# Kernel tuning notes

Hardware: AMD Instinct MI355X
Metric: run time of the kernel (lower is better)

## Reference

```python
import jax, jax.numpy as jnp
import numpy as np

E = 8            # num_experts
PS = 8           # patch size (fixed across layers since ps-2 < 8)
F = 6            # fourier frequencies
CC = 4 + 8 * F   # coord feature channels = 52
RH = 16          # router hidden channels (embed_dim)
TEMP = 1.0
THRESH = 0.05
LAYERS = [(3, 8), (8, 16), (16, 16), (16, 32)]  # (C_in, C_out) per layer
NUM_CLASSES = 100


def coord_features(H, W, ps, nf):
    # [4+8F, H, W]: global (x,y) + patch-local (x,y) + sin/cos fourier bands
    gy = (jnp.arange(H, dtype=jnp.float32) + 0.5) / H
    gx = (jnp.arange(W, dtype=jnp.float32) + 0.5) / W
    ly = ((jnp.arange(H) % ps).astype(jnp.float32) + 0.5) / ps
    lx = ((jnp.arange(W) % ps).astype(jnp.float32) + 0.5) / ps
    Gy = jnp.broadcast_to(gy[:, None], (H, W))
    Gx = jnp.broadcast_to(gx[None, :], (H, W))
    Ly = jnp.broadcast_to(ly[:, None], (H, W))
    Lx = jnp.broadcast_to(lx[None, :], (H, W))
    base = jnp.stack([Gx, Gy, Lx, Ly], 0)  # [4,H,W]
    bands = [base]
    for f in range(nf):
        w = (2.0 ** f) * jnp.pi
        bands.append(jnp.sin(w * base))
        bands.append(jnp.cos(w * base))
    return jnp.concatenate(bands, 0)


def patchify(x, ps):
    B, C, H, W = x.shape
    h, w = H // ps, W // ps
    x = x.reshape(B, C, h, ps, w, ps).transpose(0, 2, 4, 1, 3, 5)
    return x.reshape(B, h * w, C, ps, ps), h, w


def unpatchify(x, h, w):
    # 'b (h w) c ph pw -> b c (h ph) (w pw)'
    B, P, C, ph, pw = x.shape
    return x.reshape(B, h, w, C, ph, pw).transpose(0, 3, 1, 4, 2, 5).reshape(B, C, h * ph, w * pw)


def pce_layer(X, ew, eb, rw, rb, rlw, rlb):
    B, C, H, W = X.shape
    Xp, h, w = patchify(X, PS)             # [B,P,C,ps,ps]
    P = h * w
    Xf = Xp.reshape(B * P, C, PS, PS)
    coords = coord_features(H, W, PS, F)   # [CC,H,W] (same for every image)
    Cp, _, _ = patchify(coords[None], PS)
    Cp = Cp[0]                             # [P,CC,ps,ps]
    # Router: 1x1 conv proj -> ReLU -> global avg pool -> linear -> softmax/temp -> threshold + renorm
    z = jax.nn.relu(jnp.einsum('rc,pcij->prij', rw, Cp) + rb[None, :, None, None])
    z = z.mean((2, 3))                     # [P,RH]
    logits = z @ rlw.T + rlb               # [P,E]
    probs = jax.nn.softmax(logits / TEMP, axis=-1)
    keep = (probs >= THRESH).astype(probs.dtype)
    probs = probs * keep
    probs = probs / (probs.sum(-1, keepdims=True) + 1e-9)
    scores = jnp.broadcast_to(probs[None], (B, P, E))  # [B,P,E]
    # Dense all-experts conv: stack experts along output channels of one conv
    y = jax.lax.conv_general_dilated(Xf, ew, (1, 1), 'SAME',
                                     dimension_numbers=('NCHW', 'OIHW', 'NCHW'))
    y = jax.nn.relu(y + eb[None, :, None, None])       # [B*P, E*Cout, ps, ps]
    Cout = ew.shape[0] // E
    y = y.reshape(B, P, E, Cout, PS, PS)
    out = jnp.einsum('bpecij,bpe->bpcij', y, scores)   # weighted combine over experts
    return unpatchify(out, h, w)


def setup_inputs() -> dict:
    key = jax.random.key(0)
    ks = jax.random.split(key, 32)
    d = {'X': jax.random.normal(ks[0], (16, 3, 128, 128), dtype=jnp.float32)}
    ki = 1
    for li, (cin, cout) in enumerate(LAYERS):
        d[f'ew{li}'] = jax.random.normal(ks[ki], (E * cout, cin, 3, 3), dtype=jnp.float32) * (1.0 / np.sqrt(cin * 9)); ki += 1
        d[f'eb{li}'] = jax.random.normal(ks[ki], (E * cout,), dtype=jnp.float32) * 0.01; ki += 1
        d[f'rw{li}'] = jax.random.normal(ks[ki], (RH, CC), dtype=jnp.float32) * (1.0 / np.sqrt(CC)); ki += 1
        d[f'rb{li}'] = jax.random.normal(ks[ki], (RH,), dtype=jnp.float32) * 0.01; ki += 1
        d[f'rlw{li}'] = jax.random.normal(ks[ki], (E, RH), dtype=jnp.float32) * (1.0 / np.sqrt(RH)); ki += 1
        d[f'rlb{li}'] = jax.random.normal(ks[ki], (E,), dtype=jnp.float32) * 0.01; ki += 1
    d['fcw'] = jax.random.normal(ks[ki], (NUM_CLASSES, LAYERS[-1][1] * 8 * 8), dtype=jnp.float32) * 0.02; ki += 1
    d['fcb'] = jnp.zeros((NUM_CLASSES,), dtype=jnp.float32)
    return d


def reference(X, ew0, eb0, rw0, rb0, rlw0, rlb0,
              ew1, eb1, rw1, rb1, rlw1, rlb1,
              ew2, eb2, rw2, rb2, rlw2, rlb2,
              ew3, eb3, rw3, rb3, rlw3, rlb3,
              fcw, fcb):
    layer_params = [(ew0, eb0, rw0, rb0, rlw0, rlb0),
                    (ew1, eb1, rw1, rb1, rlw1, rlb1),
                    (ew2, eb2, rw2, rb2, rlw2, rlb2),
                    (ew3, eb3, rw3, rb3, rlw3, rlb3)]
    for p in layer_params:
        X = pce_layer(X, *p)
    B, C, H, W = X.shape
    # AdaptiveAvgPool2d(8): exact 16x16 mean pooling for 128x128
    pooled = X.reshape(B, C, 8, H // 8, 8, W // 8).mean((3, 5))
    flat = pooled.reshape(B, -1)
    return flat @ fcw.T + fcb
```

## Files before the change

kernel.cpp:

```cpp
#include <hip/hip_runtime.h>
#include <math.h>

#define NE 8
#define PI_F 3.14159265358979323846f

typedef _Float16 half8 __attribute__((ext_vector_type(8)));
typedef float f32x4 __attribute__((ext_vector_type(4)));
typedef unsigned int uint2v __attribute__((ext_vector_type(2)));
typedef unsigned int u32x4 __attribute__((ext_vector_type(4)));
typedef unsigned short u16x4 __attribute__((ext_vector_type(4)));

#define CP 24
#define ROWS 240
#define NELEM 2400

__device__ __forceinline__ unsigned short f2h_bits(float v) {
    union { _Float16 h; unsigned short u; } cv;
    cv.h = (_Float16)v;
    return cv.u;
}

struct SetupArgs {
    const float* rw[4]; const float* rb[4]; const float* rlw[4]; const float* rlb[4];
    const float* ew[4];
    float* probs;
    unsigned short* w0; unsigned short* w1; unsigned short* w2; unsigned short* w3;
};

template<int CIN, int COUT_R, int COUT_P, int CSTR, int KS>
__device__ __forceinline__ void prep_one(
    const float* __restrict__ ew, unsigned short* __restrict__ wA, int idx)
{
    int j    = idx & 7;
    int lane = (idx >> 3) & 63;
    int t2   = idx >> 9;
    int ks   = t2 % KS;
    int mt   = t2 / KS;
    int m    = mt * 16 + (lane & 15);
    int e    = m / COUT_P, row = m % COUT_P;
    int k    = ks * 32 + (lane >> 4) * 8 + j;
    int cin  = k % CSTR, r = k / CSTR;
    float val = 0.0f;
    if (row < COUT_R && cin < CIN && r < 9)
        val = ew[((size_t)(e * COUT_R + row) * CIN + cin) * 9 + r];
    wA[idx] = f2h_bits(val);
}

__global__ __launch_bounds__(256) void setup_all(SetupArgs sa)
{
    int bx = blockIdx.x, tid = threadIdx.x;
    if (bx < 256) {
        int layer = tid >> 6, lane = tid & 63;
        const float* rw  = sa.rw[layer];  const float* rb  = sa.rb[layer];
        const float* rlw = sa.rlw[layer]; const float* rlb = sa.rlb[layer];
        int p = bx, py = p >> 4, px = p & 15;
        int i = lane >> 3, j = lane & 7;
        int y = py * 8 + i, x = px * 8 + j;

        float base0 = (x + 0.5f) / 128.0f;
        float base1 = (y + 0.5f) / 128.0f;
        float base2 = (j + 0.5f) / 8.0f;
        float base3 = (i + 0.5f) / 8.0f;

        float coord[52];
        coord[0] = base0; coord[1] = base1; coord[2] = base2; coord[3] = base3;
        int c = 4;
        #pragma unroll
        for (int f = 0; f < 6; ++f) {
            float w = PI_F * (float)(1 << f);
            coord[c+0] = sinf(w * base0); coord[c+1] = sinf(w * base1);
            coord[c+2] = sinf(w * base2); coord[c+3] = sinf(w * base3);
            coord[c+4] = cosf(w * base0); coord[c+5] = cosf(w * base1);
            coord[c+6] = cosf(w * base2); coord[c+7] = cosf(w * base3);
            c += 8;
        }
        float z[16];
        #pragma unroll
        for (int r = 0; r < 16; ++r) {
            float a = rb[r];
            #pragma unroll
            for (int cc = 0; cc < 52; ++cc) a += rw[r*52 + cc] * coord[cc];
            z[r] = fmaxf(a, 0.0f);
        }
        #pragma unroll
        for (int r = 0; r < 16; ++r) {
            float v = z[r];
            #pragma unroll
            for (int off = 32; off > 0; off >>= 1) v += __shfl_xor(v, off);
            z[r] = v * (1.0f / 64.0f);
        }
        int e = lane & 7;
        float logit = rlb[e];
        #pragma unroll
        for (int r = 0; r < 16; ++r) logit += rlw[e*16 + r] * z[r];
        float m = logit;
        #pragma unroll
        for (int off = 4; off > 0; off >>= 1) m = fmaxf(m, __shfl_xor(m, off));
        float ex = expf(logit - m);
        float s = ex;
        #pragma unroll
        for (int off = 4; off > 0; off >>= 1) s += __shfl_xor(s, off);
        float pr = ex / s;
        pr = (pr >= 0.05f) ? pr : 0.0f;
        float s2 = pr;
        #pragma unroll
        for (int off = 4; off > 0; off >>= 1) s2 += __shfl_xor(s2, off);
        pr = pr / (s2 + 1e-9f);
        if (lane < 8) sa.probs[layer * 2048 + p * 8 + lane] = pr;
    } else {
        int idx = (bx - 256) * 256 + tid;
        if (idx < 8192)       prep_one<3, 8, 16, 4, 2>(sa.ew[0], sa.w0, idx);
        else if (idx < 20480) prep_one<8, 16, 16, 8, 3>(sa.ew[1], sa.w1, idx - 8192);
        else if (idx < 40960) prep_one<16, 16, 16, 16, 5>(sa.ew[2], sa.w2, idx - 20480);
        else if (idx < 81920) prep_one<16, 32, 32, 16, 5>(sa.ew[3], sa.w3, idx - 40960);
    }
}

template<int KS, int CSTR>
__device__ __forceinline__ void build_B(
    half8* B, const unsigned short* ain, int pr, int pc, int lane4)
{
    const int rbase = pr * ROWS + pc * CP;
    if (CSTR == 16) {
        int cb = (lane4 & 1) * 8;
        int rb = lane4 >> 1;
        #pragma unroll
        for (int ks = 0; ks < KS; ++ks) {
            int r0 = 2 * ks, r1 = 2 * ks + 1;
            int o0 = ((r0 / 3) * 10 + (r0 % 3)) * CP;
            int o1 = ((r1 / 3) * 10 + (r1 % 3)) * CP;
            int off = rb ? o1 : o0;
            half8 v{};
            if (2 * ks + rb < 9) v = *(const half8*)(ain + rbase + off + cb);
            B[ks] = v;
        }
    } else if (CSTR == 8) {
        #pragma unroll
        for (int ks = 0; ks < KS; ++ks) {
            int r = 4 * ks + lane4;
            int dy = (r * 11) >> 5, dx = r - 3 * dy;
            half8 v{};
            if (r < 9) v = *(const half8*)(ain + rbase + (dy * 10 + dx) * CP);
            B[ks] = v;
        }
    } else {
        #pragma unroll
        for (int ks = 0; ks < KS; ++ks) {
            union { half8 v; uint2v u2[2]; } bb;
            #pragma unroll
            for (int h = 0; h < 2; ++h) {
                int r = 8 * ks + 2 * lane4 + h;
                int dy = (r * 11) >> 5, dx = r - 3 * dy;
                uint2v u{};
                if (r < 9) u = *(const uint2v*)(ain + rbase + (dy * 10 + dx) * CP);
                bb.u2[h] = u;
            }
            B[ks] = bb.v;
        }
    }
}

template<int KS, int CSTR, int MT, int MPE, bool LAST>
__device__ __forceinline__ void layer_run2(
    const unsigned short* ain, unsigned short* aout,
    const unsigned short* __restrict__ wA,
    const float* sbL, const float* seL,
    int lane4, int row4,
    int pr0, int pc0, int pr1, int pc1,
    float (*ps)[32], int w, int l)
{
    half8 B0[KS], B1[KS];
    build_B<KS, CSTR>(B0, ain, pr0, pc0, lane4);
    build_B<KS, CSTR>(B1, ain, pr1, pc1, lane4);

    f32x4 acc00 = {0.f,0.f,0.f,0.f};
    f32x4 acc01 = {0.f,0.f,0.f,0.f};
    f32x4 acc10 = {0.f,0.f,0.f,0.f};
    f32x4 acc11 = {0.f,0.f,0.f,0.f};

    const unsigned short* apl = wA + l * 8;
    half8 Aa[KS], Ab[KS];
    #pragma unroll
    for (int ks = 0; ks < KS; ++ks)
        Aa[ks] = *(const half8*)(apl + ks * 512);

    #pragma unroll 1
    for (int mt = 0; mt < MT; mt += 2) {
        #pragma unroll
        for (int ks = 0; ks < KS; ++ks)
            Ab[ks] = *(const half8*)(apl + ((mt + 1) * KS + ks) * 512);

        {
            float pe = seL[(MPE == 2) ? (mt >> 1) : mt];
            f32x4 c0 = *(const f32x4*)&sbL[mt * 16 + row4];
            f32x4 c1 = c0;
            #pragma unroll
            for (int ks = 0; ks < KS; ++ks) {
                c0 = __builtin_amdgcn_mfma_f32_16x16x32_f16(Aa[ks], B0[ks], c0, 0, 0, 0);
                c1 = __builtin_amdgcn_mfma_f32_16x16x32_f16(Aa[ks], B1[ks], c1, 0, 0, 0);
            }
            #pragma unroll
            for (int j = 0; j < 4; ++j) {
                acc00[j] = fmaf(fmaxf(c0[j], 0.0f), pe, acc00[j]);
                acc10[j] = fmaf(fmaxf(c1[j], 0.0f), pe, acc10[j]);
            }
        }

        int mtn = (mt + 2 < MT) ? (mt + 2) : 0;
        #pragma unroll
        for (int ks = 0; ks < KS; ++ks)
            Aa[ks] = *(const half8*)(apl + (mtn * KS + ks) * 512);

        {
            float pe = seL[(MPE == 2) ? (mt >> 1) : (mt + 1)];
            f32x4 c0 = *(const f32x4*)&sbL[(mt + 1) * 16 + row4];
            f32x4 c1 = c0;
            #pragma unroll
            for (int ks = 0; ks < KS; ++ks) {
                c0 = __builtin_amdgcn_mfma_f32_16x16x32_f16(Ab[ks], B0[ks], c0, 0, 0, 0);
                c1 = __builtin_amdgcn_mfma_f32_16x16x32_f16(Ab[ks], B1[ks], c1, 0, 0, 0);
            }
            #pragma unroll
            for (int j = 0; j < 4; ++j) {
                if (MPE == 2) {
                    acc01[j] = fmaf(fmaxf(c0[j], 0.0f), pe, acc01[j]);
                    acc11[j] = fmaf(fmaxf(c1[j], 0.0f), pe, acc11[j]);
                } else {
                    acc00[j] = fmaf(fmaxf(c0[j], 0.0f), pe, acc00[j]);
                    acc10[j] = fmaf(fmaxf(c1[j], 0.0f), pe, acc10[j]);
                }
            }
        }
    }

    if (!LAST) {
        const int wbase0 = (1 + pr0) * ROWS + (1 + pc0) * CP;
        const int wbase1 = (1 + pr1) * ROWS + (1 + pc1) * CP;
        union { _Float16 h[4]; u16x4 u; } o0, o1;
        #pragma unroll
        for (int j = 0; j < 4; ++j) {
            o0.h[j] = (_Float16)acc00[j];
            o1.h[j] = (_Float16)acc10[j];
        }
        *(u16x4*)(aout + wbase0 + row4) = o0.u;
        *(u16x4*)(aout + wbase1 + row4) = o1.u;
    } else {
        #pragma unroll
        for (int j = 0; j < 4; ++j) {
            float s0 = acc00[j] + acc10[j];
            float s1 = acc01[j] + acc11[j];
            #pragma unroll
            for (int off = 1; off < 16; off <<= 1) {
                s0 += __shfl_xor(s0, off);
                s1 += __shfl_xor(s1, off);
            }
            if ((l & 15) == 0) {
                ps[w][row4 + j] = s0;
                ps[w][16 + row4 + j] = s1;
            }
        }
    }
}

__global__ __launch_bounds__(256, 4) void pce_fused(
    const float* __restrict__ X,
    const unsigned short* __restrict__ wA0, const unsigned short* __restrict__ wA1,
    const unsigned short* __restrict__ wA2, const unsigned short* __restrict__ wA3,
    const float* __restrict__ eb0, const float* __restrict__ eb1,
    const float* __restrict__ eb2, const float* __restrict__ eb3,
    const float* __restrict__ probs,
    float* __restrict__ psums)
{
    int bx = blockIdx.x;
    int b = bx >> 7;
    int pp = (bx & 127) << 1;
    int tid = threadIdx.x;

    __shared__ alignas(16) unsigned short A0[2][NELEM];
    __shared__ alignas(16) unsigned short A1[2][NELEM];
    __shared__ alignas(16) float sb[640];
    __shared__ alignas(16) float se[4][2][8];
    __shared__ float ps[4][32];

    {
        u32x4 z = {0u, 0u, 0u, 0u};
        for (int t = tid; t < 600; t += 256) {
            ((u32x4*)A0)[t] = z;
            ((u32x4*)A1)[t] = z;
        }
    }
    if (tid < 64) {
        int layer = tid >> 4, q = (tid >> 3) & 1, e = tid & 7;
        se[layer][q][e] = probs[layer * 2048 + (pp + q) * 8 + e];
    }
    for (int t = tid; t < 640; t += 256) {
        float v;
        if (t < 128)      { int e = t >> 4, r = t & 15; v = (r < 8) ? eb0[e * 8 + r] : 0.0f; }
        else if (t < 256) v = eb1[t - 128];
        else if (t < 384) v = eb2[t - 256];
        else              v = eb3[t - 384];
        sb[t] = v;
    }
    __syncthreads();

    for (int t = tid; t < 384; t += 256) {
        int q = t / 192, r = t - q * 192;
        int cin = r >> 6, pix = r & 63, i = pix >> 3, j = pix & 7;
        int p = pp + q, py = p >> 4, px = p & 15;
        float v = X[((size_t)(b * 3 + cin) * 128 + (py * 8 + i)) * 128 + (px * 8 + j)];
        A0[q][(1 + i) * ROWS + (1 + j) * CP + cin] = f2h_bits(v);
    }
    __syncthreads();

    int l = tid & 63, w = tid >> 6;
    int q = w >> 1;
    int n0 = (w & 1) * 32 + (l & 15), n1 = n0 + 16;
    int pr0 = n0 >> 3, pc0 = n0 & 7;
    int pr1 = n1 >> 3, pc1 = n1 & 7;
    int lane4 = l >> 4, row4 = lane4 * 4;

    layer_run2<2, 4, 8, 1, false>(A0[q], A1[q], wA0, sb,       se[0][q], lane4, row4, pr0, pc0, pr1, pc1, nullptr, w, l);
    __syncthreads();
    layer_run2<3, 8, 8, 1, false>(A1[q], A0[q], wA1, sb + 128, se[1][q], lane4, row4, pr0, pc0, pr1, pc1, nullptr, w, l);
    __syncthreads();
    layer_run2<5, 16, 8, 1, false>(A0[q], A1[q], wA2, sb + 256, se[2][q], lane4, row4, pr0, pc0, pr1, pc1, nullptr, w, l);
    __syncthreads();
    layer_run2<5, 16, 16, 2, true>(A1[q], A0[q], wA3, sb + 384, se[3][q], lane4, row4, pr0, pc0, pr1, pc1, ps, w, l);
    __syncthreads();

    if (tid < 64) {
        int qq = tid >> 5, c = tid & 31;
        psums[(size_t)(b * 256 + pp + qq) * 32 + c] = ps[2 * qq][c] + ps[2 * qq + 1][c];
    }
}

__global__ __launch_bounds__(256) void fc_kernel(
    const float* __restrict__ psums, const float* __restrict__ fcw,
    const float* __restrict__ fcb, float* __restrict__ out)
{
    int b = blockIdx.x >> 3, chunk = blockIdx.x & 7;
    __shared__ float pooled[2048];
    for (int t = threadIdx.x; t < 2048; t += 256) {
        int c = t >> 6, cell = t & 63, oy = cell >> 3, ox = cell & 7;
        float s = 0.0f;
        #pragma unroll
        for (int dy = 0; dy < 2; ++dy)
            #pragma unroll
            for (int dx = 0; dx < 2; ++dx) {
                int pp = (2 * oy + dy) * 16 + (2 * ox + dx);
                s += psums[(size_t)(b * 256 + pp) * 32 + c];
            }
        pooled[t] = s * (1.0f / 256.0f);
    }
    __syncthreads();

    int wave = threadIdx.x >> 6, lane = threadIdx.x & 63;
    for (int ci = wave; ci < 13; ci += 4) {
        int cls = chunk * 13 + ci;
        if (cls < 100) {
            float a = 0.0f;
            #pragma unroll
            for (int r = 0; r < 32; ++r)
                a += pooled[r * 64 + lane] * fcw[(size_t)cls * 2048 + r * 64 + lane];
            #pragma unroll
            for (int off = 32; off > 0; off >>= 1) a += __shfl_down(a, off);
            if (lane == 0) out[b * 100 + cls] = a + fcb[cls];
        }
    }
}

extern "C" void kernel_launch(void* const* d_in, const int* in_sizes, int n_in,
                              void* d_out, int out_size, void* d_ws, size_t ws_size,
                              hipStream_t stream) {
    const float* X = (const float*)d_in[0];
    const float* eb[4];
    SetupArgs sa;
    for (int l = 0; l < 4; ++l) {
        sa.ew[l]  = (const float*)d_in[1 + 6*l + 0];
        eb[l]     = (const float*)d_in[1 + 6*l + 1];
        sa.rw[l]  = (const float*)d_in[1 + 6*l + 2];
        sa.rb[l]  = (const float*)d_in[1 + 6*l + 3];
        sa.rlw[l] = (const float*)d_in[1 + 6*l + 4];
        sa.rlb[l] = (const float*)d_in[1 + 6*l + 5];
    }
    const float* fcw = (const float*)d_in[25];
    const float* fcb = (const float*)d_in[26];

    char* ws = (char*)d_ws;
    float* probs  = (float*)ws;
    float* psums  = (float*)(ws + 32768);
    unsigned short* wA0 = (unsigned short*)(ws + 32768 + 524288);
    unsigned short* wA1 = wA0 + 8192;
    unsigned short* wA2 = wA1 + 12288;
    unsigned short* wA3 = wA2 + 20480;

    sa.probs = probs; sa.w0 = wA0; sa.w1 = wA1; sa.w2 = wA2; sa.w3 = wA3;

    setup_all<<<576, 256, 0, stream>>>(sa);
    pce_fused<<<2048, 256, 0, stream>>>(X, wA0, wA1, wA2, wA3,
                                        eb[0], eb[1], eb[2], eb[3], probs, psums);
    fc_kernel<<<128, 256, 0, stream>>>(psums, fcw, fcb, (float*)d_out);
}
```

Measured before the change: 79.60 us.

## Assign one wavefront per patch with in-place LDS buffer and no block barriers

Remaps work so each wavefront owns a whole 8x8 patch and computes all four 16-pixel N-tiles, instead of two wavefronts splitting a patch across ping-pong buffers. Each wavefront keeps a single LDS buffer that it reads into registers and then overwrites in place, so the __syncthreads between layers go away. Each weight fragment loaded is now reused across four MFMA tiles, and the final patch sums go straight to global memory. In exchange, register pressure rises (launch bounds relaxed to 2) and the grid is halved, leaving fewer waves in flight.

```diff
diff --git a/kernel.cpp b/kernel.cpp
--- a/kernel.cpp
+++ b/kernel.cpp
@@ -160,23 +160,45 @@
     }
 }
 
+template<int KS, int MPE>
+__device__ __forceinline__ void tile_step(
+    const half8* Ax, const half8 (*B)[KS],
+    const float* sbL, const float* seL, int mt, int row4, f32x4* acc)
+{
+    float pe = seL[(MPE == 2) ? (mt >> 1) : mt];
+    f32x4 bias = *(const f32x4*)&sbL[mt * 16 + row4];
+    f32x4 c0 = bias, c1 = bias, c2 = bias, c3 = bias;
+    #pragma unroll
+    for (int ks = 0; ks < KS; ++ks) {
+        c0 = __builtin_amdgcn_mfma_f32_16x16x32_f16(Ax[ks], B[0][ks], c0, 0, 0, 0);
+        c1 = __builtin_amdgcn_mfma_f32_16x16x32_f16(Ax[ks], B[1][ks], c1, 0, 0, 0);
+        c2 = __builtin_amdgcn_mfma_f32_16x16x32_f16(Ax[ks], B[2][ks], c2, 0, 0, 0);
+        c3 = __builtin_amdgcn_mfma_f32_16x16x32_f16(Ax[ks], B[3][ks], c3, 0, 0, 0);
+    }
+    #pragma unroll
+    for (int j = 0; j < 4; ++j) {
+        acc[0][j] = fmaf(fmaxf(c0[j], 0.0f), pe, acc[0][j]);
+        acc[1][j] = fmaf(fmaxf(c1[j], 0.0f), pe, acc[1][j]);
+        acc[2][j] = fmaf(fmaxf(c2[j], 0.0f), pe, acc[2][j]);
+        acc[3][j] = fmaf(fmaxf(c3[j], 0.0f), pe, acc[3][j]);
+    }
+}
+
 template<int KS, int CSTR, int MT, int MPE, bool LAST>
-__device__ __forceinline__ void layer_run2(
-    const unsigned short* ain, unsigned short* aout,
+__device__ __forceinline__ void layer_run4(
+    unsigned short* Aw,
     const unsigned short* __restrict__ wA,
     const float* sbL, const float* seL,
-    int lane4, int row4,
-    int pr0, int pc0, int pr1, int pc1,
-    float (*ps)[32], int w, int l)
-{
-    half8 B0[KS], B1[KS];
-    build_B<KS, CSTR>(B0, ain, pr0, pc0, lane4);
-    build_B<KS, CSTR>(B1, ain, pr1, pc1, lane4);
-
-    f32x4 acc00 = {0.f,0.f,0.f,0.f};
-    f32x4 acc01 = {0.f,0.f,0.f,0.f};
-    f32x4 acc10 = {0.f,0.f,0.f,0.f};
-    f32x4 acc11 = {0.f,0.f,0.f,0.f};
+    int l, int lane4, int row4, int prb, int pc0,
+    float* pout)
+{
+    half8 B[4][KS];
+    #pragma unroll
+    for (int n = 0; n < 4; ++n)
+        build_B<KS, CSTR>(B[n], Aw, 2 * n + prb, pc0, lane4);
+
+    f32x4 acc0[4] = {{0,0,0,0},{0,0,0,0},{0,0,0,0},{0,0,0,0}};
+    f32x4 acc1[4] = {{0,0,0,0},{0,0,0,0},{0,0,0,0},{0,0,0,0}};
 
     const unsigned short* apl = wA + l * 8;
     half8 Aa[KS], Ab[KS];
@@ -190,79 +212,45 @@
         for (int ks = 0; ks < KS; ++ks)
             Ab[ks] = *(const half8*)(apl + ((mt + 1) * KS + ks) * 512);
 
-        {
-            float pe = seL[(MPE == 2) ? (mt >> 1) : mt];
-            f32x4 c0 = *(const f32x4*)&sbL[mt * 16 + row4];
-            f32x4 c1 = c0;
-            #pragma unroll
-            for (int ks = 0; ks < KS; ++ks) {
-                c0 = __builtin_amdgcn_mfma_f32_16x16x32_f16(Aa[ks], B0[ks], c0, 0, 0, 0);
-                c1 = __builtin_amdgcn_mfma_f32_16x16x32_f16(Aa[ks], B1[ks], c1, 0, 0, 0);
-            }
-            #pragma unroll
-            for (int j = 0; j < 4; ++j) {
-                acc00[j] = fmaf(fmaxf(c0[j], 0.0f), pe, acc00[j]);
-                acc10[j] = fmaf(fmaxf(c1[j], 0.0f), pe, acc10[j]);
-            }
-        }
+        tile_step<KS, MPE>(Aa, B, sbL, seL, mt, row4, acc0);
 
         int mtn = (mt + 2 < MT) ? (mt + 2) : 0;
         #pragma unroll
         for (int ks = 0; ks < KS; ++ks)
             Aa[ks] = *(const half8*)(apl + (mtn * KS + ks) * 512);
 
-        {
-            float pe = seL[(MPE == 2) ? (mt >> 1) : (mt + 1)];
-            f32x4 c0 = *(const f32x4*)&sbL[(mt + 1) * 16 + row4];
-            f32x4 c1 = c0;
-            #pragma unroll
-            for (int ks = 0; ks < KS; ++ks) {
-                c0 = __builtin_amdgcn_mfma_f32_16x16x32_f16(Ab[ks], B0[ks], c0, 0, 0, 0);
-                c1 = __builtin_amdgcn_mfma_f32_16x16x32_f16(Ab[ks], B1[ks], c1, 0, 0, 0);
-            }
-            #pragma unroll
-            for (int j = 0; j < 4; ++j) {
-                if (MPE == 2) {
-                    acc01[j] = fmaf(fmaxf(c0[j], 0.0f), pe, acc01[j]);
-                    acc11[j] = fmaf(fmaxf(c1[j], 0.0f), pe, acc11[j]);
-                } else {
-                    acc00[j] = fmaf(fmaxf(c0[j], 0.0f), pe, acc00[j]);
-                    acc10[j] = fmaf(fmaxf(c1[j], 0.0f), pe, acc10[j]);
-                }
-            }
-        }
+        tile_step<KS, MPE>(Ab, B, sbL, seL, mt + 1, row4,
+                           (MPE == 2) ? acc1 : acc0);
     }
 
     if (!LAST) {
-        const int wbase0 = (1 + pr0) * ROWS + (1 + pc0) * CP;
-        const int wbase1 = (1 + pr1) * ROWS + (1 + pc1) * CP;
-        union { _Float16 h[4]; u16x4 u; } o0, o1;
+        #pragma unroll
+        for (int n = 0; n < 4; ++n) {
+            int wbase = (1 + 2 * n + prb) * ROWS + (1 + pc0) * CP;
+            union { _Float16 h[4]; u16x4 u; } o;
+            #pragma unroll
+            for (int j = 0; j < 4; ++j) o.h[j] = (_Float16)acc0[n][j];
+            *(u16x4*)(Aw + wbase + row4) = o.u;
+        }
+    } else {
         #pragma unroll
         for (int j = 0; j < 4; ++j) {
-            o0.h[j] = (_Float16)acc00[j];
-            o1.h[j] = (_Float16)acc10[j];
-        }
-        *(u16x4*)(aout + wbase0 + row4) = o0.u;
-        *(u16x4*)(aout + wbase1 + row4) = o1.u;
-    } else {
-        #pragma unroll
-        for (int j = 0; j < 4; ++j) {
-            float s0 = acc00[j] + acc10[j];
-            float s1 = acc01[j] + acc11[j];
+            float s0 = acc0[0][j] + acc0[1][j] + acc0[2][j] + acc0[3][j];
+            float s1 = acc1[0][j] + acc1[1][j] + acc1[2][j] + acc1[3][j];
             #pragma unroll
             for (int off = 1; off < 16; off <<= 1) {
                 s0 += __shfl_xor(s0, off);
                 s1 += __shfl_xor(s1, off);
             }
             if ((l & 15) == 0) {
-                ps[w][row4 + j] = s0;
-                ps[w][16 + row4 + j] = s1;
+                pout[row4 + j] = s0;
+                pout[16 + row4 + j] = s1;
             }
         }
     }
 }
 
-__global__ __launch_bounds__(256, 4) void pce_fused(
+__global__ __launch_bounds__(256, 2) void pce_fused(
     const float* __restrict__ X,
     const unsigned short* __restrict__ wA0, const unsigned short* __restrict__ wA1,
     const unsigned short* __restrict__ wA2, const unsigned short* __restrict__ wA3,
@@ -272,26 +260,20 @@
     float* __restrict__ psums)
 {
     int bx = blockIdx.x;
-    int b = bx >> 7;
-    int pp = (bx & 127) << 1;
+    int b = bx >> 6;
+    int pbase = (bx & 63) << 2;
     int tid = threadIdx.x;
-
-    __shared__ alignas(16) unsigned short A0[2][NELEM];
-    __shared__ alignas(16) unsigned short A1[2][NELEM];
+    int w = tid >> 6, l = tid & 63;
+    int p = pbase + w;
+    int py = p >> 4, px = p & 15;
+
+    __shared__ alignas(16) unsigned short A[4][NELEM];
     __shared__ alignas(16) float sb[640];
-    __shared__ alignas(16) float se[4][2][8];
-    __shared__ float ps[4][32];
-
-    {
-        u32x4 z = {0u, 0u, 0u, 0u};
-        for (int t = tid; t < 600; t += 256) {
-            ((u32x4*)A0)[t] = z;
-            ((u32x4*)A1)[t] = z;
-        }
-    }
-    if (tid < 64) {
-        int layer = tid >> 4, q = (tid >> 3) & 1, e = tid & 7;
-        se[layer][q][e] = probs[layer * 2048 + (pp + q) * 8 + e];
+    __shared__ alignas(16) float se[4][4][8];
+
+    if (tid < 128) {
+        int layer = tid >> 5, q = (tid >> 3) & 3, e = tid & 7;
+        se[layer][q][e] = probs[layer * 2048 + (pbase + q) * 8 + e];
     }
     for (int t = tid; t < 640; t += 256) {
         float v;
@@ -301,37 +283,29 @@
         else              v = eb3[t - 384];
         sb[t] = v;
     }
+
+    unsigned short* Aw = A[w];
+    {
+        u32x4 z = {0u, 0u, 0u, 0u};
+        for (int t = l; t < 300; t += 64) ((u32x4*)Aw)[t] = z;
+        for (int t = l; t < 192; t += 64) {
+            int cin = t >> 6, pix = t & 63, i = pix >> 3, j = pix & 7;
+            float v = X[((size_t)(b * 3 + cin) * 128 + (py * 8 + i)) * 128 + (px * 8 + j)];
+            Aw[(1 + i) * ROWS + (1 + j) * CP + cin] = f2h_bits(v);
+        }
+    }
     __syncthreads();
 
-    for (int t = tid; t < 384; t += 256) {
-        int q = t / 192, r = t - q * 192;
-        int cin = r >> 6, pix = r & 63, i = pix >> 3, j = pix & 7;
-        int p = pp + q, py = p >> 4, px = p & 15;
-        float v = X[((size_t)(b * 3 + cin) * 128 + (py * 8 + i)) * 128 + (px * 8 + j)];
-        A0[q][(1 + i) * ROWS + (1 + j) * CP + cin] = f2h_bits(v);
-    }
-    __syncthreads();
-
-    int l = tid & 63, w = tid >> 6;
-    int q = w >> 1;
-    int n0 = (w & 1) * 32 + (l & 15), n1 = n0 + 16;
-    int pr0 = n0 >> 3, pc0 = n0 & 7;
-    int pr1 = n1 >> 3, pc1 = n1 & 7;
     int lane4 = l >> 4, row4 = lane4 * 4;
-
-    layer_run2<2, 4, 8, 1, false>(A0[q], A1[q], wA0, sb,       se[0][q], lane4, row4, pr0, pc0, pr1, pc1, nullptr, w, l);
-    __syncthreads();
-    layer_run2<3, 8, 8, 1, false>(A1[q], A0[q], wA1, sb + 128, se[1][q], lane4, row4, pr0, pc0, pr1, pc1, nullptr, w, l);
-    __syncthreads();
-    layer_run2<5, 16, 8, 1, false>(A0[q], A1[q], wA2, sb + 256, se[2][q], lane4, row4, pr0, pc0, pr1, pc1, nullptr, w, l);
-    __syncthreads();
-    layer_run2<5, 16, 16, 2, true>(A1[q], A0[q], wA3, sb + 384, se[3][q], lane4, row4, pr0, pc0, pr1, pc1, ps, w, l);
-    __syncthreads();
-
-    if (tid < 64) {
-        int qq = tid >> 5, c = tid & 31;
-        psums[(size_t)(b * 256 + pp + qq) * 32 + c] = ps[2 * qq][c] + ps[2 * qq + 1][c];
-    }
+    int pix0 = l & 15;
+    int prb = pix0 >> 3, pc0 = pix0 & 7;
+
+    float* pout = psums + (size_t)(b * 256 + p) * 32;
+
+    layer_run4<2, 4, 8, 1, false>(Aw, wA0, sb,       se[0][w], l, lane4, row4, prb, pc0, nullptr);
+    layer_run4<3, 8, 8, 1, false>(Aw, wA1, sb + 128, se[1][w], l, lane4, row4, prb, pc0, nullptr);
+    layer_run4<5, 16, 8, 1, false>(Aw, wA2, sb + 256, se[2][w], l, lane4, row4, prb, pc0, nullptr);
+    layer_run4<5, 16, 16, 2, true>(Aw, wA3, sb + 384, se[3][w], l, lane4, row4, prb, pc0, pout);
 }
 
 __global__ __launch_bounds__(256) void fc_kernel(
@@ -397,7 +371,7 @@
     sa.probs = probs; sa.w0 = wA0; sa.w1 = wA1; sa.w2 = wA2; sa.w3 = wA3;
 
     setup_all<<<576, 256, 0, stream>>>(sa);
-    pce_fused<<<2048, 256, 0, stream>>>(X, wA0, wA1, wA2, wA3,
+    pce_fused<<<1024, 256, 0, stream>>>(X, wA0, wA1, wA2, wA3,
                                         eb[0], eb[1], eb[2], eb[3], probs, psums);
     fc_kernel<<<128, 256, 0, stream>>>(psums, fcw, fcb, (float*)d_out);
 }
```

Result: no change. 80.83 us (+1.5%).
